# Kernel tuning notes

Measured on AMD Instinct MI355X. Metric: run time of the kernel, lower is better.

The kernel has to match this reference:

```python
import jax, jax.numpy as jnp
import numpy as np

# --- static config (matches init_kwargs) ---
B = 2; HI = 60; WI = 60; T = 4; WS = 8; SHIFT = 4
C = 256; NH = 8; HD = C // NH; HID = 1024
P = HI * WI; N = T * P
PAD = (WS - HI % WS) % WS           # 4 -> pad 60 -> 64
HP = HI + PAD; WP = WI + PAD
NWH = HP // WS; NWW = WP // WS
L = WS * WS                          # 64 tokens per window
SCALE = HD ** -0.5

# relative position index [L, L] (constant)
_c = np.stack(np.meshgrid(np.arange(WS), np.arange(WS), indexing='ij')).reshape(2, -1)
_r = (_c[:, :, None] - _c[:, None, :]).transpose(1, 2, 0) + WS - 1
REL_IDX = jnp.asarray(_r[..., 0] * (2 * WS - 1) + _r[..., 1])

# per-window key padding mask [nWin, L] (True = padded token)
_b = np.zeros((HP, WP), bool); _b[HI:, :] = True; _b[:, WI:] = True
WIN_MASK = jnp.asarray(_b.reshape(NWH, WS, NWW, WS).transpose(0, 2, 1, 3).reshape(NWH * NWW, L))


def _ln(x, w, b):
    m = x.mean(-1, keepdims=True)
    v = jnp.square(x - m).mean(-1, keepdims=True)
    return (x - m) * jax.lax.rsqrt(v + 1e-5) * w + b


def _partition(x4):  # [Bm, HP, WP, C] -> [Bm*nWin, L, C]
    Bm = x4.shape[0]
    return x4.reshape(Bm, NWH, WS, NWW, WS, C).transpose(0, 1, 3, 2, 4, 5).reshape(Bm * NWH * NWW, L, C)


def _win_attn(xq, xkv, qw, qb, kw, kb, vw, vb, ow, ob, bias_table):
    Bm = B * T
    q4 = xq.reshape(Bm, HI, WI, C)
    k4 = xkv.reshape(Bm, HI, WI, C)
    q4 = jnp.roll(q4, (-SHIFT, -SHIFT), (1, 2))
    k4 = jnp.roll(k4, (-SHIFT, -SHIFT), (1, 2))
    pad = ((0, 0), (0, PAD), (0, PAD), (0, 0))
    q4 = jnp.pad(q4, pad); k4 = jnp.pad(k4, pad)
    q_win = _partition(q4)   # [Bw, L, C]
    kv_win = _partition(k4)
    q = (q_win @ qw.T + qb).reshape(-1, L, NH, HD)
    k = (kv_win @ kw.T + kb).reshape(-1, L, NH, HD)
    v = (kv_win @ vw.T + vb).reshape(-1, L, NH, HD)
    attn = jnp.einsum('bihd,bjhd->bhij', q, k) * SCALE
    attn = attn + bias_table[REL_IDX].transpose(2, 0, 1)[None]      # RPB [1,H,L,L]
    km = jnp.tile(WIN_MASK, (Bm, 1))                                  # [Bw, L]
    attn = jnp.where(km[:, None, None, :], -jnp.inf, attn)
    p = jax.nn.softmax(attn, axis=-1)
    o = jnp.einsum('bhij,bjhd->bihd', p, v).reshape(-1, L, C)
    o = o @ ow.T + ob
    y = o.reshape(Bm, NWH, NWW, WS, WS, C).transpose(0, 1, 3, 2, 4, 5).reshape(Bm, HP, WP, C)
    y = y[:, :HI, :WI, :]
    y = jnp.roll(y, (SHIFT, SHIFT), (1, 2))
    return y.reshape(B, N, C)


def reference(x, context, ln1_w, ln1_b, ln2_w, ln2_b, ln3_w, ln3_b, lnc_w, lnc_b,
              sa_q_w, sa_q_b, sa_k_w, sa_k_b, sa_v_w, sa_v_b, sa_o_w, sa_o_b, sa_bias,
              ca_q_w, ca_q_b, ca_k_w, ca_k_b, ca_v_w, ca_v_b, ca_o_w, ca_o_b, ca_bias,
              gamma1, gamma2, gamma_mlp, mlp_w1, mlp_b1, mlp_w2, mlp_b2):
    xn = _ln(x, ln1_w, ln1_b)
    y_s = _win_attn(xn, xn, sa_q_w, sa_q_b, sa_k_w, sa_k_b, sa_v_w, sa_v_b, sa_o_w, sa_o_b, sa_bias)
    x = x + gamma1 * y_s
    y_c = _win_attn(_ln(x, ln2_w, ln2_b), _ln(context, lnc_w, lnc_b),
                    ca_q_w, ca_q_b, ca_k_w, ca_k_b, ca_v_w, ca_v_b, ca_o_w, ca_o_b, ca_bias)
    x = x + gamma2 * y_c
    h = _ln(x, ln3_w, ln3_b)
    h = jax.nn.gelu(h @ mlp_w1.T + mlp_b1, approximate=False) @ mlp_w2.T + mlp_b2
    return x + gamma_mlp * h


def setup_inputs() -> dict:
    key = jax.random.key(0)
    ks = jax.random.split(key, 16)
    def w(k, shape, s=0.02):
        return jax.random.normal(k, shape, jnp.float32) * s
    inp = {}
    inp['x'] = jax.random.normal(ks[0], (B, N, C), jnp.float32)
    inp['context'] = jax.random.normal(ks[1], (B, N, C), jnp.float32)
    for nm in ['ln1', 'ln2', 'ln3', 'lnc']:
        inp[f'{nm}_w'] = jnp.ones((C,), jnp.float32)
        inp[f'{nm}_b'] = jnp.zeros((C,), jnp.float32)
    i = 2
    for pfx in ['sa', 'ca']:
        for pn in ['q', 'k', 'v', 'o']:
            inp[f'{pfx}_{pn}_w'] = w(ks[i], (C, C)); i += 1
            inp[f'{pfx}_{pn}_b'] = jnp.zeros((C,), jnp.float32)
        inp[f'{pfx}_bias'] = w(ks[i], ((2 * WS - 1) * (2 * WS - 1), NH)); i += 1
    inp['gamma1'] = jnp.ones((1,), jnp.float32)
    inp['gamma2'] = jnp.ones((1,), jnp.float32)
    inp['gamma_mlp'] = jnp.full((1,), 0.1, jnp.float32)
    inp['mlp_w1'] = w(ks[i], (HID, C)); i += 1
    inp['mlp_b1'] = jnp.zeros((HID,), jnp.float32)
    inp['mlp_w2'] = w(ks[i], (C, HID)); i += 1
    inp['mlp_b2'] = jnp.zeros((C,), jnp.float32)
    return inp
```

## Files before the change

### kernel.cpp

```cpp
#include <hip/hip_runtime.h>
#include <math.h>

#define BN    28800
#define CC    256
#define HIDN  1024
#define WINS  512
#define WROWS (WINS*64)
#define ATT_SCALE 0.1767766952966369f

typedef __bf16 bf16x8 __attribute__((ext_vector_type(8)));
typedef float  f32x4  __attribute__((ext_vector_type(4)));

__device__ __forceinline__ unsigned short f2bf(float f) {
    unsigned u = __float_as_uint(f);
    unsigned r = (u + 0x7FFFu + ((u >> 16) & 1u)) >> 16;
    return (unsigned short)r;
}
__device__ __forceinline__ float bf2f(unsigned short u) {
    return __uint_as_float((unsigned)u << 16);
}

__device__ __forceinline__ float gelu_f(float x) {
    float x3 = x * x * x;
    float e  = __expf(1.5957691216057308f * (x + 0.044715f * x3));
    float th = 1.0f - 2.0f / (e + 1.0f);
    return 0.5f * x * (1.0f + th);
}

__device__ __forceinline__ void gl_lds16(const void* g, void* l) {
    __builtin_amdgcn_global_load_lds(
        (const __attribute__((address_space(1))) void*)g,
        (__attribute__((address_space(3))) void*)l, 16, 0, 0);
}

__global__ void ln_kernel(const float* __restrict__ x, const float* __restrict__ w,
                          const float* __restrict__ b, unsigned short* __restrict__ out, int ntok) {
    int tok  = (int)((blockIdx.x * blockDim.x + threadIdx.x) >> 6);
    int lane = threadIdx.x & 63;
    if (tok >= ntok) return;
    float4 v = reinterpret_cast<const float4*>(x + (size_t)tok * CC)[lane];
    float s  = v.x + v.y + v.z + v.w;
    float s2 = v.x*v.x + v.y*v.y + v.z*v.z + v.w*v.w;
#pragma unroll
    for (int off = 32; off >= 1; off >>= 1) {
        s  += __shfl_xor(s, off);
        s2 += __shfl_xor(s2, off);
    }
    float mean = s * (1.0f / CC);
    float var  = s2 * (1.0f / CC) - mean * mean;
    float rs   = rsqrtf(var + 1e-5f);
    float4 wv = reinterpret_cast<const float4*>(w)[lane];
    float4 bv = reinterpret_cast<const float4*>(b)[lane];
    ushort4 o;
    o.x = f2bf((v.x - mean) * rs * wv.x + bv.x);
    o.y = f2bf((v.y - mean) * rs * wv.y + bv.y);
    o.z = f2bf((v.z - mean) * rs * wv.z + bv.z);
    o.w = f2bf((v.w - mean) * rs * wv.w + bv.w);
    reinterpret_cast<ushort4*>(out + (size_t)tok * CC)[lane] = o;
}

__global__ void ln_gather(const float* __restrict__ x, const float* __restrict__ w,
                          const float* __restrict__ b, unsigned short* __restrict__ dst) {
    int row  = (int)((blockIdx.x * blockDim.x + threadIdx.x) >> 6);
    int lane = threadIdx.x & 63;
    if (row >= WROWS) return;
    int win = row >> 6, l = row & 63;
    int f   = win >> 6;
    int wih = (win >> 3) & 7, wiw = win & 7;
    int r = l >> 3, s = l & 7;
    int h = wih * 8 + r, wc = wiw * 8 + s;
    if (h >= 60 || wc >= 60) {
        ushort4 z = {0, 0, 0, 0};
        reinterpret_cast<ushort4*>(dst + (size_t)row * CC)[lane] = z;
        return;
    }
    int oh = (h + 4) % 60, ow = (wc + 4) % 60;
    size_t tok = (size_t)f * 3600 + (size_t)oh * 60 + ow;
    float4 v = reinterpret_cast<const float4*>(x + tok * CC)[lane];
    float sm  = v.x + v.y + v.z + v.w;
    float s2 = v.x*v.x + v.y*v.y + v.z*v.z + v.w*v.w;
#pragma unroll
    for (int off = 32; off >= 1; off >>= 1) {
        sm += __shfl_xor(sm, off);
        s2 += __shfl_xor(s2, off);
    }
    float mean = sm * (1.0f / CC);
    float var  = s2 * (1.0f / CC) - mean * mean;
    float rs   = rsqrtf(var + 1e-5f);
    float4 wv = reinterpret_cast<const float4*>(w)[lane];
    float4 bv = reinterpret_cast<const float4*>(b)[lane];
    ushort4 o;
    o.x = f2bf((v.x - mean) * rs * wv.x + bv.x);
    o.y = f2bf((v.y - mean) * rs * wv.y + bv.y);
    o.z = f2bf((v.z - mean) * rs * wv.z + bv.z);
    o.w = f2bf((v.w - mean) * rs * wv.w + bv.w);
    reinterpret_cast<ushort4*>(dst + (size_t)row * CC)[lane] = o;
}

__device__ __forceinline__ void stage_tile(const unsigned short* __restrict__ Wt,
                                           const unsigned short* __restrict__ Act,
                                           int m0, int n0, int K, int k0,
                                           unsigned short* dA, unsigned short* dB,
                                           int t, int w) {
#pragma unroll
    for (int p = 0; p < 2; ++p) {
        int c   = p * 256 + t;
        int row = c >> 2;
        int gl  = (c & 3) ^ ((row >> 1) & 3);
        gl_lds16(Wt  + (size_t)(m0 + row) * K + k0 + gl * 8,
                 (char*)dA + (p * 256 + w * 64) * 16);
        gl_lds16(Act + (size_t)(n0 + row) * K + k0 + gl * 8,
                 (char*)dB + (p * 256 + w * 64) * 16);
    }
}

template <bool GELU, int FUSE>
__global__ __launch_bounds__(256) void gemm_wa(
        const unsigned short* __restrict__ Wt,
        const unsigned short* __restrict__ Act,
        const float* __restrict__ b0, const float* __restrict__ b1,
        const float* __restrict__ b2, const float* __restrict__ b3,
        unsigned short* __restrict__ o0, unsigned short* __restrict__ o1,
        unsigned short* __restrict__ o2, unsigned short* __restrict__ o3,
        int strideO, int vseg, int K,
        const float* __restrict__ xres, const float* __restrict__ gammap,
        float* __restrict__ fout) {
    __shared__ __align__(16) char pool[32768];
    unsigned short* A0 = (unsigned short*)pool;
    unsigned short* B0 = (unsigned short*)(pool + 8192);
    unsigned short* A1 = (unsigned short*)(pool + 16384);
    unsigned short* B1 = (unsigned short*)(pool + 24576);
    unsigned short* Cs = (unsigned short*)pool;

    const int t = threadIdx.x;
    const int w = t >> 6, l = t & 63;
    const int Mb = gridDim.x;
    int lin = blockIdx.y * Mb + blockIdx.x;
    int T = Mb * gridDim.y;
    int q = T >> 3, rr = T & 7;
    int xcd = lin & 7, slot = lin >> 3;
    int wid = (xcd < rr) ? (xcd * (q + 1) + slot)
                         : (rr * (q + 1) + (xcd - rr) * q + slot);
    const int m0 = (wid % Mb) * 128;
    const int n0 = (wid / Mb) * 128;

    const int wr = w >> 1, wc = w & 1;
    const int r = l & 15, g = l >> 4;
    const int sw = (r >> 1) & 3;
    const int gp = (g ^ sw) * 8;
    f32x4 acc[4][4];
#pragma unroll
    for (int i = 0; i < 4; ++i)
#pragma unroll
        for (int j = 0; j < 4; ++j) { acc[i][j][0]=0.f; acc[i][j][1]=0.f; acc[i][j][2]=0.f; acc[i][j][3]=0.f; }

    stage_tile(Wt, Act, m0, n0, K, 0,  A0, B0, t, w);
    stage_tile(Wt, Act, m0, n0, K, 32, A1, B1, t, w);
    const int nt = K >> 5;
    for (int kt = 0; kt < nt; ++kt) {
        if (kt < nt - 1)
            asm volatile("s_waitcnt vmcnt(4)" ::: "memory");
        else
            asm volatile("s_waitcnt vmcnt(0)" ::: "memory");
        __builtin_amdgcn_s_barrier();
        __builtin_amdgcn_sched_barrier(0);
        const unsigned short* cA = (kt & 1) ? A1 : A0;
        const unsigned short* cB = (kt & 1) ? B1 : B0;
        bf16x8 af[4], bw[4];
#pragma unroll
        for (int m = 0; m < 4; ++m)
            af[m] = *reinterpret_cast<const bf16x8*>(&cA[(wr * 64 + m * 16 + r) * 32 + gp]);
#pragma unroll
        for (int n = 0; n < 4; ++n)
            bw[n] = *reinterpret_cast<const bf16x8*>(&cB[(wc * 64 + n * 16 + r) * 32 + gp]);
#pragma unroll
        for (int m = 0; m < 4; ++m)
#pragma unroll
            for (int n = 0; n < 4; ++n)
                acc[m][n] = __builtin_amdgcn_mfma_f32_16x16x32_bf16(af[m], bw[n], acc[m][n], 0, 0, 0);
        __builtin_amdgcn_sched_barrier(0);
        asm volatile("s_waitcnt lgkmcnt(0)" ::: "memory");
        __builtin_amdgcn_s_barrier();
        __builtin_amdgcn_sched_barrier(0);
        if (kt + 2 < nt) {
            unsigned short* sA = (kt & 1) ? A1 : A0;
            unsigned short* sB = (kt & 1) ? B1 : B0;
            stage_tile(Wt, Act, m0, n0, K, (kt + 2) * 32, sA, sB, t, w);
        }
    }

    const int seg = m0 >> 8;
    const float* bp = (seg == 0) ? b0 : (seg == 1) ? b1 : (seg == 2) ? b2 : b3;
    unsigned short* op = (seg == 0) ? o0 : (seg == 1) ? o1 : (seg == 2) ? o2 : o3;
    const int chseg = m0 & 255;

    if (FUSE == 0 && seg == vseg) {
#pragma unroll
        for (int m = 0; m < 4; ++m) {
            const int ch0 = chseg + wr * 64 + m * 16 + g * 4;
            float4 b4 = *reinterpret_cast<const float4*>(bp + ch0);
            const float bb[4] = {b4.x, b4.y, b4.z, b4.w};
#pragma unroll
            for (int n = 0; n < 4; ++n) {
                const int tok = n0 + wc * 64 + n * 16 + r;
#pragma unroll
                for (int j = 0; j < 4; ++j)
                    op[(size_t)(ch0 + j) * 32768 + tok] = f2bf(acc[m][n][j] + bb[j]);
            }
        }
        return;
    }

#pragma unroll
    for (int m = 0; m < 4; ++m) {
        const int ch0 = wr * 64 + m * 16 + g * 4;
        float4 b4 = *reinterpret_cast<const float4*>(bp + chseg + ch0);
        const float bb[4] = {b4.x, b4.y, b4.z, b4.w};
#pragma unroll
        for (int n = 0; n < 4; ++n) {
            const int tok_l = wc * 64 + n * 16 + r;
            float cv[4];
#pragma unroll
            for (int j = 0; j < 4; ++j) {
                cv[j] = acc[m][n][j] + bb[j];
                if (GELU) cv[j] = gelu_f(cv[j]);
            }
            ushort4 pk;
            pk.x = f2bf(cv[0]); pk.y = f2bf(cv[1]); pk.z = f2bf(cv[2]); pk.w = f2bf(cv[3]);
            int gran = (ch0 >> 2) ^ ((tok_l & 15) << 1);
            reinterpret_cast<ushort4*>(Cs)[tok_l * 32 + gran] = pk;
        }
    }
    __syncthreads();
    const int u = t & 15, trow = t >> 4;
    if (FUSE == 0) {
#pragma unroll
        for (int it = 0; it < 8; ++it) {
            int tok_l = it * 16 + trow;
            int up = u ^ (tok_l & 15);
            uint4 v = reinterpret_cast<const uint4*>(Cs)[tok_l * 16 + up];
            *reinterpret_cast<uint4*>(op + (size_t)(n0 + tok_l) * strideO + chseg + u * 8) = v;
        }
    } else {
        const float gsc = gammap[0];
#pragma unroll
        for (int it = 0; it < 8; ++it) {
            int tok_l = it * 16 + trow;
            int wrow = n0 + tok_l;
            int tok;
            if (FUSE == 1) {
                int win = wrow >> 6, l2 = wrow & 63;
                int f = win >> 6, wih = (win >> 3) & 7, wiw = win & 7;
                int r2 = l2 >> 3, s2 = l2 & 7;
                int h = wih * 8 + r2, wcol = wiw * 8 + s2;
                if (h >= 60 || wcol >= 60) continue;
                int oh = h + 4; if (oh >= 60) oh -= 60;
                int ow = wcol + 4; if (ow >= 60) ow -= 60;
                tok = f * 3600 + oh * 60 + ow;
            } else {
                tok = wrow;
            }
            int up = u ^ (tok_l & 15);
            uint4 v = reinterpret_cast<const uint4*>(Cs)[tok_l * 16 + up];
            const unsigned short* pu = (const unsigned short*)&v;
            const float* xr = xres + (size_t)tok * CC + chseg + u * 8;
            float4 xa = *reinterpret_cast<const float4*>(xr);
            float4 xb = *reinterpret_cast<const float4*>(xr + 4);
            float4 oa, ob;
            oa.x = xa.x + gsc * bf2f(pu[0]);
            oa.y = xa.y + gsc * bf2f(pu[1]);
            oa.z = xa.z + gsc * bf2f(pu[2]);
            oa.w = xa.w + gsc * bf2f(pu[3]);
            ob.x = xb.x + gsc * bf2f(pu[4]);
            ob.y = xb.y + gsc * bf2f(pu[5]);
            ob.z = xb.z + gsc * bf2f(pu[6]);
            ob.w = xb.w + gsc * bf2f(pu[7]);
            float* fo = fout + (size_t)tok * CC + chseg + u * 8;
            *reinterpret_cast<float4*>(fo) = oa;
            *reinterpret_cast<float4*>(fo + 4) = ob;
        }
    }
}

__global__ void expand_bias(const float* __restrict__ sa, const float* __restrict__ ca,
                            float* __restrict__ dst) {
    int e = (int)(blockIdx.x * blockDim.x + threadIdx.x);
    const float* src = (e < 16384) ? sa : ca;
    int e2 = e & 16383;
    int h = e2 >> 12, ij = e2 & 4095, i = ij >> 6, j = ij & 63;
    int ri = i >> 3, si = i & 7, rj = j >> 3, sj = j & 7;
    dst[e] = src[((ri - rj + 7) * 15 + (si - sj + 7)) * 8 + h];
}

__global__ __launch_bounds__(256) void attn_mfma(
        const unsigned short* __restrict__ Q,
        const unsigned short* __restrict__ K,
        const unsigned short* __restrict__ VT,
        const float* __restrict__ biasx,
        unsigned short* __restrict__ AO) {
    __shared__ __align__(16) unsigned short Pl[4][64 * 64];
    const int t = threadIdx.x;
    const int w = t >> 6, l = t & 63;
    const int win = blockIdx.x >> 1;
    const int h   = (blockIdx.x & 1) * 4 + w;
    const int c = l & 15, g = l >> 4;
    const int wih = (win >> 3) & 7, wiw = win & 7;
    const size_t qkbase = (size_t)win * 64 * CC + (size_t)h * 32;

    bf16x8 ka[4], qb[4];
#pragma unroll
    for (int mj = 0; mj < 4; ++mj)
        ka[mj] = *reinterpret_cast<const bf16x8*>(K + qkbase + (size_t)(mj * 16 + c) * CC + g * 8);
#pragma unroll
    for (int ni = 0; ni < 4; ++ni)
        qb[ni] = *reinterpret_cast<const bf16x8*>(Q + qkbase + (size_t)(ni * 16 + c) * CC + g * 8);
    f32x4 s[4][4];
#pragma unroll
    for (int mj = 0; mj < 4; ++mj)
#pragma unroll
        for (int ni = 0; ni < 4; ++ni) { s[mj][ni][0]=0.f; s[mj][ni][1]=0.f; s[mj][ni][2]=0.f; s[mj][ni][3]=0.f; }
#pragma unroll
    for (int mj = 0; mj < 4; ++mj)
#pragma unroll
        for (int ni = 0; ni < 4; ++ni)
            s[mj][ni] = __builtin_amdgcn_mfma_f32_16x16x32_bf16(ka[mj], qb[ni], s[mj][ni], 0, 0, 0);

    const float* bx = biasx + h * 4096;
    const bool modd = (wiw == 7) && (g & 1);
#pragma unroll
    for (int mj = 0; mj < 4; ++mj) {
        const bool mmj = (wih == 7) && (mj >= 2);
#pragma unroll
        for (int ni = 0; ni < 4; ++ni) {
            float4 b4 = *reinterpret_cast<const float4*>(bx + (ni * 16 + c) * 64 + mj * 16 + g * 4);
            const float bb[4] = {b4.x, b4.y, b4.z, b4.w};
#pragma unroll
            for (int jj = 0; jj < 4; ++jj) {
                float v = s[mj][ni][jj] * ATT_SCALE + bb[jj];
                s[mj][ni][jj] = (mmj || modd) ? -1e30f : v;
            }
        }
    }

#pragma unroll
    for (int ni = 0; ni < 4; ++ni) {
        float mx = -1e30f;
#pragma unroll
        for (int mj = 0; mj < 4; ++mj)
#pragma unroll
            for (int jj = 0; jj < 4; ++jj) mx = fmaxf(mx, s[mj][ni][jj]);
        mx = fmaxf(mx, __shfl_xor(mx, 16));
        mx = fmaxf(mx, __shfl_xor(mx, 32));
        float sum = 0.f;
#pragma unroll
        for (int mj = 0; mj < 4; ++mj)
#pragma unroll
            for (int jj = 0; jj < 4; ++jj) {
                float p = __expf(s[mj][ni][jj] - mx);
                s[mj][ni][jj] = p;
                sum += p;
            }
        sum += __shfl_xor(sum, 16);
        sum += __shfl_xor(sum, 32);
        float rinv = 1.0f / sum;
        const int i  = ni * 16 + c;
        const int ik = i & 7;
#pragma unroll
        for (int mj = 0; mj < 4; ++mj) {
            ushort4 pk;
            pk.x = f2bf(s[mj][ni][0] * rinv);
            pk.y = f2bf(s[mj][ni][1] * rinv);
            pk.z = f2bf(s[mj][ni][2] * rinv);
            pk.w = f2bf(s[mj][ni][3] * rinv);
            int chunk = (mj * 2 + (g >> 1)) ^ ik;
            *reinterpret_cast<ushort4*>((char*)&Pl[w][0] + i * 128 + chunk * 16 + (g & 1) * 8) = pk;
        }
    }

    bf16x8 vb[2][2];
#pragma unroll
    for (int nd = 0; nd < 2; ++nd)
#pragma unroll
        for (int kt = 0; kt < 2; ++kt)
            vb[nd][kt] = *reinterpret_cast<const bf16x8*>(
                VT + (size_t)(h * 32 + nd * 16 + c) * 32768 + win * 64 + kt * 32 + g * 8);
    f32x4 o[4][2];
#pragma unroll
    for (int mi = 0; mi < 4; ++mi)
#pragma unroll
        for (int nd = 0; nd < 2; ++nd) { o[mi][nd][0]=0.f; o[mi][nd][1]=0.f; o[mi][nd][2]=0.f; o[mi][nd][3]=0.f; }
#pragma unroll
    for (int mi = 0; mi < 4; ++mi) {
        const int i  = mi * 16 + c;
        const int ik = i & 7;
#pragma unroll
        for (int kt = 0; kt < 2; ++kt) {
            int chunk = (kt * 4 + g) ^ ik;
            bf16x8 pa = *reinterpret_cast<const bf16x8*>((char*)&Pl[w][0] + i * 128 + chunk * 16);
#pragma unroll
            for (int nd = 0; nd < 2; ++nd)
                o[mi][nd] = __builtin_amdgcn_mfma_f32_16x16x32_bf16(pa, vb[nd][kt], o[mi][nd], 0, 0, 0);
        }
    }

    unsigned short* aop = AO + qkbase;
#pragma unroll
    for (int mi = 0; mi < 4; ++mi)
#pragma unroll
        for (int nd = 0; nd < 2; ++nd)
#pragma unroll
            for (int jj = 0; jj < 4; ++jj)
                aop[(size_t)(mi * 16 + g * 4 + jj) * CC + nd * 16 + c] = f2bf(o[mi][nd][jj]);
}

__global__ void cvt_all(const float* s0, const float* s1, const float* s2, const float* s3,
                        const float* s4, const float* s5, const float* s6, const float* s7,
                        const float* s8, const float* s9, unsigned short* __restrict__ dst) {
    const float* srcs[10] = {s0, s1, s2, s3, s4, s5, s6, s7, s8, s9};
    int blk = blockIdx.x;
    int wi = (blk < 512) ? (blk >> 6) : (blk < 768 ? 8 : 9);
    size_t start = (wi < 8) ? (size_t)wi * 65536 : (wi == 8 ? (size_t)524288 : (size_t)786432);
    size_t gidx = (size_t)blk * 1024 + (size_t)threadIdx.x * 4;
    float4 v = *reinterpret_cast<const float4*>(srcs[wi] + (gidx - start));
    ushort4 o;
    o.x = f2bf(v.x); o.y = f2bf(v.y); o.z = f2bf(v.z); o.w = f2bf(v.w);
    *reinterpret_cast<ushort4*>(dst + gidx) = o;
}

extern "C" void kernel_launch(void* const* d_in, const int* in_sizes, int n_in,
                              void* d_out, int out_size, void* d_ws, size_t ws_size,
                              hipStream_t stream) {
    const float* x    = (const float*)d_in[0];
    const float* ctx  = (const float*)d_in[1];
    const float* ln1w = (const float*)d_in[2];
    const float* ln1b = (const float*)d_in[3];
    const float* ln2w = (const float*)d_in[4];
    const float* ln2b = (const float*)d_in[5];
    const float* ln3w = (const float*)d_in[6];
    const float* ln3b = (const float*)d_in[7];
    const float* lncw = (const float*)d_in[8];
    const float* lncb = (const float*)d_in[9];
    const float* saqw = (const float*)d_in[10];
    const float* saqb = (const float*)d_in[11];
    const float* sakw = (const float*)d_in[12];
    const float* sakb = (const float*)d_in[13];
    const float* savw = (const float*)d_in[14];
    const float* savb = (const float*)d_in[15];
    const float* saow = (const float*)d_in[16];
    const float* saob = (const float*)d_in[17];
    const float* sabias = (const float*)d_in[18];
    const float* caqw = (const float*)d_in[19];
    const float* caqb = (const float*)d_in[20];
    const float* cakw = (const float*)d_in[21];
    const float* cakb = (const float*)d_in[22];
    const float* cavw = (const float*)d_in[23];
    const float* cavb = (const float*)d_in[24];
    const float* caow = (const float*)d_in[25];
    const float* caob = (const float*)d_in[26];
    const float* cabias = (const float*)d_in[27];
    const float* gamma1 = (const float*)d_in[28];
    const float* gamma2 = (const float*)d_in[29];
    const float* gammam = (const float*)d_in[30];
    const float* mw1 = (const float*)d_in[31];
    const float* mb1 = (const float*)d_in[32];
    const float* mw2 = (const float*)d_in[33];
    const float* mb2 = (const float*)d_in[34];

    float* ws = (float*)d_ws;
    unsigned short* LNbf = (unsigned short*)(ws);
    unsigned short* Gq   = (unsigned short*)(ws + 3686400);
    unsigned short* Gkv  = (unsigned short*)(ws + 7880704);
    unsigned short* Qbf  = (unsigned short*)(ws + 12075008);
    unsigned short* Kbf  = (unsigned short*)(ws + 16269312);
    unsigned short* VTbf = (unsigned short*)(ws + 20463616);
    float* X1  = ws + 28852224;
    unsigned short* Wp = (unsigned short*)(ws + 36225024);
    float* biasx = ws + 36749312;
    unsigned short* AObf = Gq;
    unsigned short* H1bf = Qbf;

    unsigned short* w_saqkv = Wp;
    unsigned short* w_sao   = Wp + 196608;
    unsigned short* w_caq   = Wp + 262144;
    unsigned short* w_cakv  = Wp + 327680;
    unsigned short* w_cao   = Wp + 458752;
    unsigned short* w_m1    = Wp + 524288;
    unsigned short* w_m2    = Wp + 786432;

    float* OUT = (float*)d_out;

    dim3 blk(256);
    dim3 gLN(BN / 4);
    dim3 gGather(WROWS / 4);
    dim3 gAttn(WINS * 2);

    cvt_all<<<dim3(1024), blk, 0, stream>>>(saqw, sakw, savw, saow, caqw, cakw, cavw, caow, mw1, mw2, Wp);
    expand_bias<<<dim3(128), blk, 0, stream>>>(sabias, cabias, biasx);

    ln_gather<<<gGather, blk, 0, stream>>>(x, ln1w, ln1b, Gq);
    gemm_wa<false,0><<<dim3(6, 256), blk, 0, stream>>>(w_saqkv, Gq, saqb, sakb, savb, savb,
                                                       Qbf, Kbf, VTbf, VTbf, CC, 2, CC,
                                                       nullptr, nullptr, nullptr);
    attn_mfma<<<gAttn, blk, 0, stream>>>(Qbf, Kbf, VTbf, biasx, AObf);
    gemm_wa<false,1><<<dim3(2, 256), blk, 0, stream>>>(w_sao, AObf, saob, saob, saob, saob,
                                                       Qbf, Qbf, Qbf, Qbf, CC, -1, CC,
                                                       x, gamma1, X1);
    ln_gather<<<gGather, blk, 0, stream>>>(X1, ln2w, ln2b, Gq);
    ln_gather<<<gGather, blk, 0, stream>>>(ctx, lncw, lncb, Gkv);
    gemm_wa<false,0><<<dim3(2, 256), blk, 0, stream>>>(w_caq, Gq, caqb, caqb, caqb, caqb,
                                                       Qbf, Qbf, Qbf, Qbf, CC, -1, CC,
                                                       nullptr, nullptr, nullptr);
    gemm_wa<false,0><<<dim3(4, 256), blk, 0, stream>>>(w_cakv, Gkv, cakb, cavb, cavb, cavb,
                                                       Kbf, VTbf, VTbf, VTbf, CC, 1, CC,
                                                       nullptr, nullptr, nullptr);
    attn_mfma<<<gAttn, blk, 0, stream>>>(Qbf, Kbf, VTbf, biasx + 16384, AObf);
    gemm_wa<false,1><<<dim3(2, 256), blk, 0, stream>>>(w_cao, AObf, caob, caob, caob, caob,
                                                       Qbf, Qbf, Qbf, Qbf, CC, -1, CC,
                                                       X1, gamma2, X1);
    ln_kernel<<<gLN, blk, 0, stream>>>(X1, ln3w, ln3b, LNbf, BN);
    gemm_wa<true,0><<<dim3(8, 225), blk, 0, stream>>>(w_m1, LNbf, mb1, mb1 + 256, mb1 + 512, mb1 + 768,
                                                      H1bf, H1bf + 256, H1bf + 512, H1bf + 768,
                                                      HIDN, -1, CC, nullptr, nullptr, nullptr);
    gemm_wa<false,2><<<dim3(2, 225), blk, 0, stream>>>(w_m2, H1bf, mb2, mb2, mb2, mb2,
                                                      Qbf, Qbf, Qbf, Qbf, CC, -1, HIDN,
                                                      X1, gammam, OUT);
}
```

Baseline: 247.7 us.

## Use 512-thread blocks with 8 waves per 128x128 GEMM tile

```diff
diff --git a/kernel.cpp b/kernel.cpp
--- a/kernel.cpp
+++ b/kernel.cpp
@@ -23,7 +23,7 @@
 __device__ __forceinline__ float gelu_f(float x) {
     float x3 = x * x * x;
     float e  = __expf(1.5957691216057308f * (x + 0.044715f * x3));
-    float th = 1.0f - 2.0f / (e + 1.0f);
+    float th = 1.0f - 2.0f * __builtin_amdgcn_rcpf(e + 1.0f);
     return 0.5f * x * (1.0f + th);
 }
 
@@ -97,25 +97,8 @@
     reinterpret_cast<ushort4*>(dst + (size_t)row * CC)[lane] = o;
 }
 
-__device__ __forceinline__ void stage_tile(const unsigned short* __restrict__ Wt,
-                                           const unsigned short* __restrict__ Act,
-                                           int m0, int n0, int K, int k0,
-                                           unsigned short* dA, unsigned short* dB,
-                                           int t, int w) {
-#pragma unroll
-    for (int p = 0; p < 2; ++p) {
-        int c   = p * 256 + t;
-        int row = c >> 2;
-        int gl  = (c & 3) ^ ((row >> 1) & 3);
-        gl_lds16(Wt  + (size_t)(m0 + row) * K + k0 + gl * 8,
-                 (char*)dA + (p * 256 + w * 64) * 16);
-        gl_lds16(Act + (size_t)(n0 + row) * K + k0 + gl * 8,
-                 (char*)dB + (p * 256 + w * 64) * 16);
-    }
-}
-
 template <bool GELU, int FUSE>
-__global__ __launch_bounds__(256) void gemm_wa(
+__global__ __launch_bounds__(512, 4) void gemm_wa(
         const unsigned short* __restrict__ Wt,
         const unsigned short* __restrict__ Act,
         const float* __restrict__ b0, const float* __restrict__ b1,
@@ -133,7 +116,8 @@
     unsigned short* Cs = (unsigned short*)pool;
 
     const int t = threadIdx.x;
-    const int w = t >> 6, l = t & 63;
+    const int w = t >> 6;
+    const int l = t & 63;
     const int Mb = gridDim.x;
     int lin = blockIdx.y * Mb + blockIdx.x;
     int T = Mb * gridDim.y;
@@ -144,39 +128,48 @@
     const int m0 = (wid % Mb) * 128;
     const int n0 = (wid / Mb) * 128;
 
-    const int wr = w >> 1, wc = w & 1;
+    const int wr = w >> 2, wc = w & 3;
     const int r = l & 15, g = l >> 4;
     const int sw = (r >> 1) & 3;
     const int gp = (g ^ sw) * 8;
-    f32x4 acc[4][4];
+    const int srow = t >> 2;
+    const int sgl  = (t & 3) ^ ((srow >> 1) & 3);
+
+    f32x4 acc[4][2];
 #pragma unroll
     for (int i = 0; i < 4; ++i)
 #pragma unroll
-        for (int j = 0; j < 4; ++j) { acc[i][j][0]=0.f; acc[i][j][1]=0.f; acc[i][j][2]=0.f; acc[i][j][3]=0.f; }
-
-    stage_tile(Wt, Act, m0, n0, K, 0,  A0, B0, t, w);
-    stage_tile(Wt, Act, m0, n0, K, 32, A1, B1, t, w);
+        for (int j = 0; j < 2; ++j) { acc[i][j][0]=0.f; acc[i][j][1]=0.f; acc[i][j][2]=0.f; acc[i][j][3]=0.f; }
+
+#define STAGE(k0, dA, dB)                                                          \
+    do {                                                                           \
+        gl_lds16(Wt  + (size_t)(m0 + srow) * K + (k0) + sgl * 8, (char*)(dA) + w * 1024); \
+        gl_lds16(Act + (size_t)(n0 + srow) * K + (k0) + sgl * 8, (char*)(dB) + w * 1024); \
+    } while (0)
+
+    STAGE(0,  A0, B0);
+    STAGE(32, A1, B1);
     const int nt = K >> 5;
     for (int kt = 0; kt < nt; ++kt) {
         if (kt < nt - 1)
-            asm volatile("s_waitcnt vmcnt(4)" ::: "memory");
+            asm volatile("s_waitcnt vmcnt(2)" ::: "memory");
         else
             asm volatile("s_waitcnt vmcnt(0)" ::: "memory");
         __builtin_amdgcn_s_barrier();
         __builtin_amdgcn_sched_barrier(0);
         const unsigned short* cA = (kt & 1) ? A1 : A0;
         const unsigned short* cB = (kt & 1) ? B1 : B0;
-        bf16x8 af[4], bw[4];
+        bf16x8 af[4], bw[2];
 #pragma unroll
         for (int m = 0; m < 4; ++m)
             af[m] = *reinterpret_cast<const bf16x8*>(&cA[(wr * 64 + m * 16 + r) * 32 + gp]);
 #pragma unroll
-        for (int n = 0; n < 4; ++n)
-            bw[n] = *reinterpret_cast<const bf16x8*>(&cB[(wc * 64 + n * 16 + r) * 32 + gp]);
+        for (int n = 0; n < 2; ++n)
+            bw[n] = *reinterpret_cast<const bf16x8*>(&cB[(wc * 32 + n * 16 + r) * 32 + gp]);
 #pragma unroll
         for (int m = 0; m < 4; ++m)
 #pragma unroll
-            for (int n = 0; n < 4; ++n)
+            for (int n = 0; n < 2; ++n)
                 acc[m][n] = __builtin_amdgcn_mfma_f32_16x16x32_bf16(af[m], bw[n], acc[m][n], 0, 0, 0);
         __builtin_amdgcn_sched_barrier(0);
         asm volatile("s_waitcnt lgkmcnt(0)" ::: "memory");
@@ -185,9 +178,10 @@
         if (kt + 2 < nt) {
             unsigned short* sA = (kt & 1) ? A1 : A0;
             unsigned short* sB = (kt & 1) ? B1 : B0;
-            stage_tile(Wt, Act, m0, n0, K, (kt + 2) * 32, sA, sB, t, w);
-        }
-    }
+            STAGE((kt + 2) * 32, sA, sB);
+        }
+    }
+#undef STAGE
 
     const int seg = m0 >> 8;
     const float* bp = (seg == 0) ? b0 : (seg == 1) ? b1 : (seg == 2) ? b2 : b3;
@@ -201,8 +195,8 @@
             float4 b4 = *reinterpret_cast<const float4*>(bp + ch0);
             const float bb[4] = {b4.x, b4.y, b4.z, b4.w};
 #pragma unroll
-            for (int n = 0; n < 4; ++n) {
-                const int tok = n0 + wc * 64 + n * 16 + r;
+            for (int n = 0; n < 2; ++n) {
+                const int tok = n0 + wc * 32 + n * 16 + r;
 #pragma unroll
                 for (int j = 0; j < 4; ++j)
                     op[(size_t)(ch0 + j) * 32768 + tok] = f2bf(acc[m][n][j] + bb[j]);
@@ -217,8 +211,8 @@
         float4 b4 = *reinterpret_cast<const float4*>(bp + chseg + ch0);
         const float bb[4] = {b4.x, b4.y, b4.z, b4.w};
 #pragma unroll
-        for (int n = 0; n < 4; ++n) {
-            const int tok_l = wc * 64 + n * 16 + r;
+        for (int n = 0; n < 2; ++n) {
+            const int tok_l = wc * 32 + n * 16 + r;
             float cv[4];
 #pragma unroll
             for (int j = 0; j < 4; ++j) {
@@ -235,8 +229,8 @@
     const int u = t & 15, trow = t >> 4;
     if (FUSE == 0) {
 #pragma unroll
-        for (int it = 0; it < 8; ++it) {
-            int tok_l = it * 16 + trow;
+        for (int it = 0; it < 4; ++it) {
+            int tok_l = it * 32 + trow;
             int up = u ^ (tok_l & 15);
             uint4 v = reinterpret_cast<const uint4*>(Cs)[tok_l * 16 + up];
             *reinterpret_cast<uint4*>(op + (size_t)(n0 + tok_l) * strideO + chseg + u * 8) = v;
@@ -244,8 +238,8 @@
     } else {
         const float gsc = gammap[0];
 #pragma unroll
-        for (int it = 0; it < 8; ++it) {
-            int tok_l = it * 16 + trow;
+        for (int it = 0; it < 4; ++it) {
+            int tok_l = it * 32 + trow;
             int wrow = n0 + tok_l;
             int tok;
             if (FUSE == 1) {
@@ -362,7 +356,7 @@
             }
         sum += __shfl_xor(sum, 16);
         sum += __shfl_xor(sum, 32);
-        float rinv = 1.0f / sum;
+        float rinv = __builtin_amdgcn_rcpf(sum);
         const int i  = ni * 16 + c;
         const int ik = i & 7;
 #pragma unroll
@@ -490,6 +484,7 @@
     float* OUT = (float*)d_out;
 
     dim3 blk(256);
+    dim3 blk512(512);
     dim3 gLN(BN / 4);
     dim3 gGather(WROWS / 4);
     dim3 gAttn(WINS * 2);
@@ -498,30 +493,30 @@
     expand_bias<<<dim3(128), blk, 0, stream>>>(sabias, cabias, biasx);
 
     ln_gather<<<gGather, blk, 0, stream>>>(x, ln1w, ln1b, Gq);
-    gemm_wa<false,0><<<dim3(6, 256), blk, 0, stream>>>(w_saqkv, Gq, saqb, sakb, savb, savb,
-                                                       Qbf, Kbf, VTbf, VTbf, CC, 2, CC,
-                                                       nullptr, nullptr, nullptr);
+    gemm_wa<false,0><<<dim3(6, 256), blk512, 0, stream>>>(w_saqkv, Gq, saqb, sakb, savb, savb,
+                                                          Qbf, Kbf, VTbf, VTbf, CC, 2, CC,
+                                                          nullptr, nullptr, nullptr);
     attn_mfma<<<gAttn, blk, 0, stream>>>(Qbf, Kbf, VTbf, biasx, AObf);
-    gemm_wa<false,1><<<dim3(2, 256), blk, 0, stream>>>(w_sao, AObf, saob, saob, saob, saob,
-                                                       Qbf, Qbf, Qbf, Qbf, CC, -1, CC,
-                                                       x, gamma1, X1);
+    gemm_wa<false,1><<<dim3(2, 256), blk512, 0, stream>>>(w_sao, AObf, saob, saob, saob, saob,
+                                                          Qbf, Qbf, Qbf, Qbf, CC, -1, CC,
+                                                          x, gamma1, X1);
     ln_gather<<<gGather, blk, 0, stream>>>(X1, ln2w, ln2b, Gq);
     ln_gather<<<gGather, blk, 0, stream>>>(ctx, lncw, lncb, Gkv);
-    gemm_wa<false,0><<<dim3(2, 256), blk, 0, stream>>>(w_caq, Gq, caqb, caqb, caqb, caqb,
-                                                       Qbf, Qbf, Qbf, Qbf, CC, -1, CC,
-                                                       nullptr, nullptr, nullptr);
-    gemm_wa<false,0><<<dim3(4, 256), blk, 0, stream>>>(w_cakv, Gkv, cakb, cavb, cavb, cavb,
-                                                       Kbf, VTbf, VTbf, VTbf, CC, 1, CC,
-                                                       nullptr, nullptr, nullptr);
+    gemm_wa<false,0><<<dim3(2, 256), blk512, 0, stream>>>(w_caq, Gq, caqb, caqb, caqb, caqb,
+                                                          Qbf, Qbf, Qbf, Qbf, CC, -1, CC,
+                                                          nullptr, nullptr, nullptr);
+    gemm_wa<false,0><<<dim3(4, 256), blk512, 0, stream>>>(w_cakv, Gkv, cakb, cavb, cavb, cavb,
+                                                          Kbf, VTbf, VTbf, VTbf, CC, 1, CC,
+                                                          nullptr, nullptr, nullptr);
     attn_mfma<<<gAttn, blk, 0, stream>>>(Qbf, Kbf, VTbf, biasx + 16384, AObf);
-    gemm_wa<false,1><<<dim3(2, 256), blk, 0, stream>>>(w_cao, AObf, caob, caob, caob, caob,
-                                                       Qbf, Qbf, Qbf, Qbf, CC, -1, CC,
-                                                       X1, gamma2, X1);
+    gemm_wa<false,1><<<dim3(2, 256), blk512, 0, stream>>>(w_cao, AObf, caob, caob, caob, caob,
+                                                          Qbf, Qbf, Qbf, Qbf, CC, -1, CC,
+                                                          X1, gamma2, X1);
     ln_kernel<<<gLN, blk, 0, stream>>>(X1, ln3w, ln3b, LNbf, BN);
-    gemm_wa<true,0><<<dim3(8, 225), blk, 0, stream>>>(w_m1, LNbf, mb1, mb1 + 256, mb1 + 512, mb1 + 768,
-                                                      H1bf, H1bf + 256, H1bf + 512, H1bf + 768,
-                                                      HIDN, -1, CC, nullptr, nullptr, nullptr);
-    gemm_wa<false,2><<<dim3(2, 225), blk, 0, stream>>>(w_m2, H1bf, mb2, mb2, mb2, mb2,
-                                                      Qbf, Qbf, Qbf, Qbf, CC, -1, HIDN,
-                                                      X1, gammam, OUT);
-}
+    gemm_wa<true,0><<<dim3(8, 225), blk512, 0, stream>>>(w_m1, LNbf, mb1, mb1 + 256, mb1 + 512, mb1 + 768,
+                                                         H1bf, H1bf + 256, H1bf + 512, H1bf + 768,
+                                                         HIDN, -1, CC, nullptr, nullptr, nullptr);
+    gemm_wa<false,2><<<dim3(2, 225), blk512, 0, stream>>>(w_m2, H1bf, mb2, mb2, mb2, mb2,
+                                                         Qbf, Qbf, Qbf, Qbf, CC, -1, HIDN,
+                                                         X1, gammam, OUT);
+}
```

New measurement: 240.5 us. 2.9% less time.

## Load GEMM weight fragments straight to registers and triple-buffer activations in LDS

Applied to the files above, without the earlier changes.

```diff
diff --git a/kernel.cpp b/kernel.cpp
--- a/kernel.cpp
+++ b/kernel.cpp
@@ -23,7 +23,7 @@
 __device__ __forceinline__ float gelu_f(float x) {
     float x3 = x * x * x;
     float e  = __expf(1.5957691216057308f * (x + 0.044715f * x3));
-    float th = 1.0f - 2.0f / (e + 1.0f);
+    float th = 1.0f - 2.0f * __builtin_amdgcn_rcpf(e + 1.0f);
     return 0.5f * x * (1.0f + th);
 }
 
@@ -97,25 +97,8 @@
     reinterpret_cast<ushort4*>(dst + (size_t)row * CC)[lane] = o;
 }
 
-__device__ __forceinline__ void stage_tile(const unsigned short* __restrict__ Wt,
-                                           const unsigned short* __restrict__ Act,
-                                           int m0, int n0, int K, int k0,
-                                           unsigned short* dA, unsigned short* dB,
-                                           int t, int w) {
-#pragma unroll
-    for (int p = 0; p < 2; ++p) {
-        int c   = p * 256 + t;
-        int row = c >> 2;
-        int gl  = (c & 3) ^ ((row >> 1) & 3);
-        gl_lds16(Wt  + (size_t)(m0 + row) * K + k0 + gl * 8,
-                 (char*)dA + (p * 256 + w * 64) * 16);
-        gl_lds16(Act + (size_t)(n0 + row) * K + k0 + gl * 8,
-                 (char*)dB + (p * 256 + w * 64) * 16);
-    }
-}
-
 template <bool GELU, int FUSE>
-__global__ __launch_bounds__(256) void gemm_wa(
+__global__ __launch_bounds__(256, 3) void gemm_wa(
         const unsigned short* __restrict__ Wt,
         const unsigned short* __restrict__ Act,
         const float* __restrict__ b0, const float* __restrict__ b1,
@@ -126,10 +109,9 @@
         const float* __restrict__ xres, const float* __restrict__ gammap,
         float* __restrict__ fout) {
     __shared__ __align__(16) char pool[32768];
-    unsigned short* A0 = (unsigned short*)pool;
-    unsigned short* B0 = (unsigned short*)(pool + 8192);
-    unsigned short* A1 = (unsigned short*)(pool + 16384);
-    unsigned short* B1 = (unsigned short*)(pool + 24576);
+    unsigned short* B0 = (unsigned short*)pool;
+    unsigned short* B1 = (unsigned short*)(pool + 8192);
+    unsigned short* B2 = (unsigned short*)(pool + 16384);
     unsigned short* Cs = (unsigned short*)pool;
 
     const int t = threadIdx.x;
@@ -148,46 +130,71 @@
     const int r = l & 15, g = l >> 4;
     const int sw = (r >> 1) & 3;
     const int gp = (g ^ sw) * 8;
+
     f32x4 acc[4][4];
 #pragma unroll
     for (int i = 0; i < 4; ++i)
 #pragma unroll
         for (int j = 0; j < 4; ++j) { acc[i][j][0]=0.f; acc[i][j][1]=0.f; acc[i][j][2]=0.f; acc[i][j][3]=0.f; }
 
-    stage_tile(Wt, Act, m0, n0, K, 0,  A0, B0, t, w);
-    stage_tile(Wt, Act, m0, n0, K, 32, A1, B1, t, w);
+#define STAGE_B(k0, dB)                                                            \
+    do {                                                                           \
+        _Pragma("unroll")                                                          \
+        for (int p = 0; p < 2; ++p) {                                              \
+            int c   = p * 256 + t;                                                 \
+            int row = c >> 2;                                                      \
+            int gl  = (c & 3) ^ ((row >> 1) & 3);                                  \
+            gl_lds16(Act + (size_t)(n0 + row) * K + (k0) + gl * 8,                 \
+                     (char*)(dB) + (p * 256 + w * 64) * 16);                       \
+        }                                                                          \
+    } while (0)
+
+#define LOAD_A(kc)                                                                 \
+    do {                                                                           \
+        _Pragma("unroll")                                                          \
+        for (int kt2 = 0; kt2 < 4; ++kt2)                                          \
+            _Pragma("unroll")                                                      \
+            for (int m = 0; m < 4; ++m)                                            \
+                afr[kt2][m] = *reinterpret_cast<const bf16x8*>(                    \
+                    Wt + (size_t)(m0 + wr * 64 + m * 16 + r) * K + (kc) + kt2 * 32 + g * 8); \
+    } while (0)
+
+    bf16x8 afr[4][4];
+    LOAD_A(0);
+    STAGE_B(0,  B0);
+    STAGE_B(32, B1);
+    STAGE_B(64, B2);
+    unsigned short *pb0 = B0, *pb1 = B1, *pb2 = B2;
     const int nt = K >> 5;
-    for (int kt = 0; kt < nt; ++kt) {
-        if (kt < nt - 1)
-            asm volatile("s_waitcnt vmcnt(4)" ::: "memory");
-        else
-            asm volatile("s_waitcnt vmcnt(0)" ::: "memory");
-        __builtin_amdgcn_s_barrier();
-        __builtin_amdgcn_sched_barrier(0);
-        const unsigned short* cA = (kt & 1) ? A1 : A0;
-        const unsigned short* cB = (kt & 1) ? B1 : B0;
-        bf16x8 af[4], bw[4];
-#pragma unroll
-        for (int m = 0; m < 4; ++m)
-            af[m] = *reinterpret_cast<const bf16x8*>(&cA[(wr * 64 + m * 16 + r) * 32 + gp]);
-#pragma unroll
-        for (int n = 0; n < 4; ++n)
-            bw[n] = *reinterpret_cast<const bf16x8*>(&cB[(wc * 64 + n * 16 + r) * 32 + gp]);
-#pragma unroll
-        for (int m = 0; m < 4; ++m)
-#pragma unroll
-            for (int n = 0; n < 4; ++n)
-                acc[m][n] = __builtin_amdgcn_mfma_f32_16x16x32_bf16(af[m], bw[n], acc[m][n], 0, 0, 0);
-        __builtin_amdgcn_sched_barrier(0);
-        asm volatile("s_waitcnt lgkmcnt(0)" ::: "memory");
-        __builtin_amdgcn_s_barrier();
-        __builtin_amdgcn_sched_barrier(0);
-        if (kt + 2 < nt) {
-            unsigned short* sA = (kt & 1) ? A1 : A0;
-            unsigned short* sB = (kt & 1) ? B1 : B0;
-            stage_tile(Wt, Act, m0, n0, K, (kt + 2) * 32, sA, sB, t, w);
-        }
-    }
+    int gs = 0;
+    for (int kc = 0; kc < K; kc += 128) {
+        if (kc) LOAD_A(kc);
+#pragma unroll
+        for (int kt2 = 0; kt2 < 4; ++kt2) {
+            if (gs < nt - 2)       asm volatile("s_waitcnt vmcnt(4)" ::: "memory");
+            else if (gs == nt - 2) asm volatile("s_waitcnt vmcnt(2)" ::: "memory");
+            else                   asm volatile("s_waitcnt vmcnt(0)" ::: "memory");
+            __builtin_amdgcn_s_barrier();
+            __builtin_amdgcn_sched_barrier(0);
+#pragma unroll
+            for (int n = 0; n < 4; ++n) {
+                bf16x8 bw = *reinterpret_cast<const bf16x8*>(&pb0[(wc * 64 + n * 16 + r) * 32 + gp]);
+#pragma unroll
+                for (int m = 0; m < 4; ++m)
+                    acc[m][n] = __builtin_amdgcn_mfma_f32_16x16x32_bf16(afr[kt2][m], bw, acc[m][n], 0, 0, 0);
+            }
+            __builtin_amdgcn_sched_barrier(0);
+            asm volatile("s_waitcnt lgkmcnt(0)" ::: "memory");
+            __builtin_amdgcn_s_barrier();
+            __builtin_amdgcn_sched_barrier(0);
+            if (gs + 3 < nt)
+                STAGE_B((gs + 3) * 32, pb0);
+            unsigned short* tmp = pb0; pb0 = pb1; pb1 = pb2; pb2 = tmp;
+            ++gs;
+        }
+    }
+#undef STAGE_B
+#undef LOAD_A
 
     const int seg = m0 >> 8;
     const float* bp = (seg == 0) ? b0 : (seg == 1) ? b1 : (seg == 2) ? b2 : b3;
@@ -362,7 +369,7 @@
             }
         sum += __shfl_xor(sum, 16);
         sum += __shfl_xor(sum, 32);
-        float rinv = 1.0f / sum;
+        float rinv = __builtin_amdgcn_rcpf(sum);
         const int i  = ni * 16 + c;
         const int ik = i & 7;
 #pragma unroll
```

Result: slower. 300.7 us (+21.4%).
